# Kernel tuning notes

Measured on AMD Instinct MI355X. Metric: run time of the kernel, lower is better.

Reference implementation:

```python
import jax, jax.numpy as jnp
import numpy as np

EPS = 1e-7  # keras.backend.epsilon()
ROUTINGS = 3


def squash(s, axis=-1):
    # standard capsule squash: ||s||^2/(1+||s||^2) * s/||s||
    n2 = jnp.sum(jnp.square(s), axis=axis, keepdims=True)
    return s * (n2 / (1.0 + n2)) / jnp.sqrt(n2 + EPS)


def setup_inputs() -> dict:
    key = jax.random.key(0)
    k1, k2 = jax.random.split(key)
    B, I, K = 32, 2048, 8          # batch, input capsules, input capsule dim
    J, D = 32, 16                  # output capsules (num_capsules), dim_capsules
    x = jax.random.normal(k1, (B, I, K), dtype=jnp.float32)
    # add_weight with random_normal_initializer(stddev=0.1), shape [J, I, D, K]
    W = 0.1 * jax.random.normal(k2, (J, I, D, K), dtype=jnp.float32)
    return {"x": x, "W": W}


def reference(x, W):
    # u_ji_hat[b,j,i,d] = sum_k W[j,i,d,k] * x[b,i,k]  (the map_fn batched matmul)
    u_hat = jnp.einsum('jidk,bik->bjid', W, x)  # [B, J, I, D]
    B, J, I, D = u_hat.shape
    b = jnp.zeros((B, J, I), dtype=u_hat.dtype)  # routing logits b_ij
    v = None
    for r in range(ROUTINGS):
        c = jax.nn.softmax(b, axis=1)                 # softmax over output capsules J
        s = jnp.einsum('bji,bjid->bjd', c, u_hat)     # weighted sum over input caps i
        v = squash(s, axis=-1)                        # squash over capsule dim (axis=-2 pre-squeeze)
        if r < ROUTINGS - 1:
            # agreement = u_hat^T v : sum over capsule dim d
            b = b + jnp.einsum('bjid,bjd->bji', u_hat, v)
    return v  # [B, J, D] == tf.squeeze(v_j, [2, 4])
```

## Files before the change

### kernel.cpp

```cpp
#include <hip/hip_runtime.h>
#include <hip/hip_fp16.h>


#define ICAP    2048
#define JD      512
#define S_ELEMS 16384
#define EPSQ    1e-7f
#define NBP     256
#define ICH     8
#define WROW    1040
#define WIL     (8 * WROW)

#define GBAR_WORDS (32 + NBP * 32)

typedef _Float16 h2v __attribute__((ext_vector_type(2)));
union H8 { int4 i4; h2v h[4]; };

#if defined(__has_builtin) && __has_builtin(__builtin_amdgcn_fdot2)
#define FDOT2(a, b, c) __builtin_amdgcn_fdot2((a), (b), (c), false)
#else
__device__ inline float FDOT2(h2v a, h2v b, float c) {
    return c + (float)a[0] * (float)b[0] + (float)a[1] * (float)b[1];
}
#endif
#if defined(__has_builtin) && __has_builtin(__builtin_amdgcn_rcpf)
#define FAST_RCP(x) __builtin_amdgcn_rcpf(x)
#else
#define FAST_RCP(x) (1.0f / (x))
#endif
#if defined(__has_builtin) && __has_builtin(__builtin_amdgcn_rsqf)
#define FAST_RSQ(x) __builtin_amdgcn_rsqf(x)
#else
#define FAST_RSQ(x) rsqrtf(x)
#endif

__device__ __forceinline__ void gsync(unsigned* gb, unsigned gen,
                                      int bid, int tid) {
    __syncthreads();
    if (tid == 0) {
        __threadfence();
        __hip_atomic_store(gb + 32 + bid * 32, gen, __ATOMIC_RELAXED,
                           __HIP_MEMORY_SCOPE_AGENT);
    }
    if (bid == 0) {
        if (tid < 64) {
            const unsigned* s = gb + 32 + tid * 32;
            for (;;) {
                bool done = true;
#pragma unroll
                for (int q = 0; q < 4; ++q) {
                    const unsigned v = __hip_atomic_load(
                        s + q * 2048, __ATOMIC_RELAXED,
                        __HIP_MEMORY_SCOPE_AGENT);
                    done &= (v >= gen);
                }
                if (__all(done)) break;
                __builtin_amdgcn_s_sleep(1);
            }
            __threadfence();
            if (tid == 0)
                __hip_atomic_store(gb, gen, __ATOMIC_RELAXED,
                                   __HIP_MEMORY_SCOPE_AGENT);
        }
    } else if (tid == 0) {
        while (__hip_atomic_load(gb, __ATOMIC_RELAXED,
                                 __HIP_MEMORY_SCOPE_AGENT) < gen)
            __builtin_amdgcn_s_sleep(8);
        __threadfence();
    }
    __syncthreads();
}

__global__ __launch_bounds__(512, 1)
void caps_fused(const float4* __restrict__ Wv, const float4* __restrict__ Xv,
                float* __restrict__ vsum, __half* __restrict__ partials,
                float* __restrict__ out, unsigned* __restrict__ gbar)
{
    __shared__ __align__(16) unsigned char sWt[WIL * ICH];
    __shared__ __align__(16) unsigned char sX[4096];
    __shared__ float rbuf[8][512];

    const int tid = threadIdx.x;
    const int bid = blockIdx.x;
    const int i0  = bid * ICH;

#pragma unroll
    for (int it = 0; it < 16; ++it) {
        const int f  = it * 512 + tid;
        const int q4 = f & 31;
        const int il = (f >> 5) & 7;
        const int jj = f >> 8;
        const float4 w = Wv[((size_t)jj * ICAP + (i0 + il)) * 32 + q4];
        ushort4 h;
        h.x = __half_as_ushort(__float2half(w.x));
        h.y = __half_as_ushort(__float2half(w.y));
        h.z = __half_as_ushort(__float2half(w.z));
        h.w = __half_as_ushort(__float2half(w.w));
        const int d   = q4 >> 1;
        const int sub = q4 & 1;
        *reinterpret_cast<ushort4*>(sWt + il * WIL + (d & 7) * WROW
                                    + (2 * jj + (d >> 3)) * 16 + sub * 8) = h;
    }
    {
        const int k4 = tid & 1, il = (tid >> 1) & 7, b = tid >> 4;
        const float4 w = Xv[((size_t)b * ICAP + (i0 + il)) * 2 + k4];
        ushort4 h;
        h.x = __half_as_ushort(__float2half(w.x));
        h.y = __half_as_ushort(__float2half(w.y));
        h.z = __half_as_ushort(__float2half(w.z));
        h.w = __half_as_ushort(__float2half(w.w));
        *reinterpret_cast<ushort4*>(sX + (b * 8 + il) * 16 + k4 * 8) = h;
    }
    __syncthreads();

    const int wave = tid >> 6, lane = tid & 63;
    const int j = lane & 31, dh = lane >> 5;
    float vacc = 0.f;

#pragma unroll
    for (int r = 0; r < 3; ++r) {
        const bool first = (r == 0);
        float vs[4][8], sacc[4][8];
#pragma unroll
        for (int bb = 0; bb < 4; ++bb) {
            const int b = wave + 8 * bb;
            if (!first) {
                const float* vp = vsum + b * JD + j * 16 + dh * 8;
                const float4 a  = *reinterpret_cast<const float4*>(vp);
                const float4 bq = *reinterpret_cast<const float4*>(vp + 4);
                vs[bb][0]=a.x; vs[bb][1]=a.y; vs[bb][2]=a.z; vs[bb][3]=a.w;
                vs[bb][4]=bq.x; vs[bb][5]=bq.y; vs[bb][6]=bq.z; vs[bb][7]=bq.w;
            }
#pragma unroll
            for (int q = 0; q < 8; ++q) sacc[bb][q] = 0.f;
        }

#pragma unroll
        for (int il = 0; il < ICH; ++il) {
            H8 w8[8];
#pragma unroll
            for (int cc = 0; cc < 8; ++cc)
                w8[cc].i4 = *reinterpret_cast<const int4*>(
                    sWt + il * WIL + cc * WROW + (2 * j + dh) * 16);
#pragma unroll
            for (int bb = 0; bb < 4; ++bb) {
                const int b = wave + 8 * bb;
                H8 xv;
                xv.i4 = *reinterpret_cast<const int4*>(sX + (b * 8 + il) * 16);

                float u[8], tpart = 0.f;
#pragma unroll
                for (int q = 0; q < 8; ++q) {
                    float acc = FDOT2(w8[q].h[0], xv.h[0], 0.f);
                    acc = FDOT2(w8[q].h[1], xv.h[1], acc);
                    acc = FDOT2(w8[q].h[2], xv.h[2], acc);
                    acc = FDOT2(w8[q].h[3], xv.h[3], acc);
                    u[q] = acc;
                    if (!first) tpart = fmaf(acc, vs[bb][q], tpart);
                }
                float c;
                if (first) {
                    c = 0.03125f;
                } else {
                    const float t = tpart + __shfl_xor(tpart, 32);
                    const float e = __expf(t);
                    float se = e;
#pragma unroll
                    for (int off = 1; off <= 16; off <<= 1)
                        se += __shfl_xor(se, off);
                    c = e * FAST_RCP(se);
                }
#pragma unroll
                for (int q = 0; q < 8; ++q)
                    sacc[bb][q] = fmaf(c, u[q], sacc[bb][q]);
            }
        }

        __half* pout = partials + (size_t)bid * S_ELEMS;
#pragma unroll
        for (int bb = 0; bb < 4; ++bb) {
            const int b = wave + 8 * bb;
            union { int4 v; __half2 h[4]; } pk;
#pragma unroll
            for (int q = 0; q < 4; ++q)
                pk.h[q] = __floats2half2_rn(sacc[bb][2 * q], sacc[bb][2 * q + 1]);
            *reinterpret_cast<int4*>(pout + b * JD + j * 16 + dh * 8) = pk.v;
        }

        gsync(gbar, 2 * r + 1, bid, tid);

        {
            const int e = bid * 64 + lane;
            float s = 0.f;
            const __half* p = partials + (size_t)wave * 32 * S_ELEMS + e;
#pragma unroll
            for (int n = 0; n < 32; ++n)
                s += __half2float(p[(size_t)n * S_ELEMS]);
            rbuf[wave][lane] = s;
            __syncthreads();
            if (wave == 0) {
                s = 0.f;
#pragma unroll
                for (int k = 0; k < 8; ++k) s += rbuf[k][lane];
                float n2 = s * s;
#pragma unroll
                for (int off = 1; off <= 8; off <<= 1)
                    n2 += __shfl_xor(n2, off);
                const float scale = n2 * FAST_RCP(1.f + n2) * FAST_RSQ(n2 + EPSQ);
                const float v = s * scale;
                if (r == 2) {
                    out[e] = v;
                } else {
                    vacc += v;
                    vsum[e] = vacc;
                }
            }
        }
        if (r < 2) gsync(gbar, 2 * r + 2, bid, tid);
    }
}

extern "C" void kernel_launch(void* const* d_in, const int* in_sizes, int n_in,
                              void* d_out, int out_size, void* d_ws, size_t ws_size,
                              hipStream_t stream) {
    const float* x = (const float*)d_in[0];
    const float* W = (const float*)d_in[1];
    float* out = (float*)d_out;

    float*    vsum     = (float*)d_ws;
    __half*   partials = (__half*)((char*)d_ws + 65536);
    unsigned* gbar     = (unsigned*)((char*)partials + (size_t)NBP * S_ELEMS * 2);

    hipMemsetAsync(gbar, 0, GBAR_WORDS * sizeof(unsigned), stream);

    caps_fused<<<NBP, 512, 0, stream>>>((const float4*)W, (const float4*)x,
                                        vsum, partials, out, gbar);
}
```

Before: 176.6 us.

## Pre-convert W to fp16 tiled layout in separate kernel; spread barrier release flags

Adds a prep kernel that converts W to fp16 and writes it in the per-block shared-memory tile layout. The fused kernel can then load its tile with contiguous int4 copies instead of strided fp32 gathers with in-kernel conversion, shortening the single-wave prologue. The grid barrier release now writes 32 separate flags, each polled by a subset of blocks, which spreads the polling traffic across cache lines. The cost is an extra kernel launch plus a full read of fp32 W and a write of the fp16 copy, and W is converted on every call.

```diff
diff --git a/kernel.cpp b/kernel.cpp
--- a/kernel.cpp
+++ b/kernel.cpp
@@ -11,7 +11,7 @@
 #define WROW    1040
 #define WIL     (8 * WROW)
 
-#define GBAR_WORDS (32 + NBP * 32)
+#define GBAR_WORDS (1024 + NBP * 32)
 
 typedef _Float16 h2v __attribute__((ext_vector_type(2)));
 union H8 { int4 i4; h2v h[4]; };
@@ -34,17 +34,42 @@
 #define FAST_RSQ(x) rsqrtf(x)
 #endif
 
+__global__ __launch_bounds__(256)
+void caps_prep(const float4* __restrict__ Wv, char* __restrict__ Wt) {
+    const int t = threadIdx.x;
+    const int i = blockIdx.x * 4 + (t >> 6);
+    const int slot = t & 63;
+    const int j = slot >> 1, dh = slot & 1;
+    const float4* src = Wv + (((size_t)j * ICAP + i) * 16 + dh * 8) * 2;
+    char* dst = Wt + ((size_t)(i >> 3) * 64 + (i & 7) * 8) * 1024 + slot * 16;
+#pragma unroll
+    for (int rr = 0; rr < 8; ++rr) {
+        const float4 a = src[rr * 2];
+        const float4 b = src[rr * 2 + 1];
+        union { int4 v; ushort u[8]; } pk;
+        pk.u[0] = __half_as_ushort(__float2half(a.x));
+        pk.u[1] = __half_as_ushort(__float2half(a.y));
+        pk.u[2] = __half_as_ushort(__float2half(a.z));
+        pk.u[3] = __half_as_ushort(__float2half(a.w));
+        pk.u[4] = __half_as_ushort(__float2half(b.x));
+        pk.u[5] = __half_as_ushort(__float2half(b.y));
+        pk.u[6] = __half_as_ushort(__float2half(b.z));
+        pk.u[7] = __half_as_ushort(__float2half(b.w));
+        *reinterpret_cast<int4*>(dst + rr * 1024) = pk.v;
+    }
+}
+
 __device__ __forceinline__ void gsync(unsigned* gb, unsigned gen,
                                       int bid, int tid) {
     __syncthreads();
     if (tid == 0) {
         __threadfence();
-        __hip_atomic_store(gb + 32 + bid * 32, gen, __ATOMIC_RELAXED,
+        __hip_atomic_store(gb + 1024 + bid * 32, gen, __ATOMIC_RELAXED,
                            __HIP_MEMORY_SCOPE_AGENT);
     }
     if (bid == 0) {
         if (tid < 64) {
-            const unsigned* s = gb + 32 + tid * 32;
+            const unsigned* s = gb + 1024 + tid * 32;
             for (;;) {
                 bool done = true;
 #pragma unroll
@@ -58,21 +83,22 @@
                 __builtin_amdgcn_s_sleep(1);
             }
             __threadfence();
-            if (tid == 0)
-                __hip_atomic_store(gb, gen, __ATOMIC_RELAXED,
+            if (tid < 32)
+                __hip_atomic_store(gb + tid * 32, gen, __ATOMIC_RELAXED,
                                    __HIP_MEMORY_SCOPE_AGENT);
         }
     } else if (tid == 0) {
-        while (__hip_atomic_load(gb, __ATOMIC_RELAXED,
+        const unsigned* flag = gb + (bid & 31) * 32;
+        while (__hip_atomic_load(flag, __ATOMIC_RELAXED,
                                  __HIP_MEMORY_SCOPE_AGENT) < gen)
-            __builtin_amdgcn_s_sleep(8);
+            __builtin_amdgcn_s_sleep(16);
         __threadfence();
     }
     __syncthreads();
 }
 
 __global__ __launch_bounds__(512, 1)
-void caps_fused(const float4* __restrict__ Wv, const float4* __restrict__ Xv,
+void caps_fused(const int4* __restrict__ Wtp, const float4* __restrict__ Xv,
                 float* __restrict__ vsum, __half* __restrict__ partials,
                 float* __restrict__ out, unsigned* __restrict__ gbar)
 {
@@ -80,26 +106,20 @@
     __shared__ __align__(16) unsigned char sX[4096];
     __shared__ float rbuf[8][512];
 
-    const int tid = threadIdx.x;
-    const int bid = blockIdx.x;
-    const int i0  = bid * ICH;
-
-#pragma unroll
-    for (int it = 0; it < 16; ++it) {
-        const int f  = it * 512 + tid;
-        const int q4 = f & 31;
-        const int il = (f >> 5) & 7;
-        const int jj = f >> 8;
-        const float4 w = Wv[((size_t)jj * ICAP + (i0 + il)) * 32 + q4];
-        ushort4 h;
-        h.x = __half_as_ushort(__float2half(w.x));
-        h.y = __half_as_ushort(__float2half(w.y));
-        h.z = __half_as_ushort(__float2half(w.z));
-        h.w = __half_as_ushort(__float2half(w.w));
-        const int d   = q4 >> 1;
-        const int sub = q4 & 1;
-        *reinterpret_cast<ushort4*>(sWt + il * WIL + (d & 7) * WROW
-                                    + (2 * jj + (d >> 3)) * 16 + sub * 8) = h;
+    const int tid  = threadIdx.x;
+    const int bid  = blockIdx.x;
+    const int i0   = bid * ICH;
+    const int wave = tid >> 6, lane = tid & 63;
+
+    {
+        const int4* wsrc = Wtp + ((size_t)bid * 65536 >> 4);
+#pragma unroll
+        for (int n = 0; n < 8; ++n) {
+            const int rid = wave * 8 + n;
+            const int il = rid >> 3, rr = rid & 7;
+            const int4 v = wsrc[(size_t)rid * 64 + lane];
+            *reinterpret_cast<int4*>(sWt + il * WIL + rr * WROW + lane * 16) = v;
+        }
     }
     {
         const int k4 = tid & 1, il = (tid >> 1) & 7, b = tid >> 4;
@@ -113,7 +133,6 @@
     }
     __syncthreads();
 
-    const int wave = tid >> 6, lane = tid & 63;
     const int j = lane & 31, dh = lane >> 5;
     float vacc = 0.f;
 
@@ -230,9 +249,12 @@
     float*    vsum     = (float*)d_ws;
     __half*   partials = (__half*)((char*)d_ws + 65536);
     unsigned* gbar     = (unsigned*)((char*)partials + (size_t)NBP * S_ELEMS * 2);
+    char*     Wtp      = (char*)gbar + GBAR_WORDS * sizeof(unsigned);
 
     hipMemsetAsync(gbar, 0, GBAR_WORDS * sizeof(unsigned), stream);
 
-    caps_fused<<<NBP, 512, 0, stream>>>((const float4*)W, (const float4*)x,
+    caps_prep<<<ICAP / 4, 256, 0, stream>>>((const float4*)W, Wtp);
+
+    caps_fused<<<NBP, 512, 0, stream>>>((const int4*)Wtp, (const float4*)x,
                                         vsum, partials, out, gbar);
 }
```

Measured after the change: 190.2 us. 7.7% more time.

## Halve block count with more input capsules per block and fan out barrier flags

Applied to the files above, without the earlier changes.

Switches from 256 blocks of 8 input capsules to 128 blocks of 16, which halves the partial-sum buffer that each routing iteration writes and then reduces across blocks. The reduction is restructured so each block sums 128 elements over 128 partials using four thread groups. The grid barrier release flag is spread over 32 cache lines so waiting blocks don't all poll one word. Partial stores and loads become nontemporal. In exchange only half the CUs are used, and shared memory per block roughly doubles, which also caps occupancy.

```diff
diff --git a/kernel.cpp b/kernel.cpp
--- a/kernel.cpp
+++ b/kernel.cpp
@@ -6,14 +6,15 @@
 #define JD      512
 #define S_ELEMS 16384
 #define EPSQ    1e-7f
-#define NBP     256
-#define ICH     8
+#define NBP     128
+#define ICH     16
 #define WROW    1040
 #define WIL     (8 * WROW)
 
-#define GBAR_WORDS (32 + NBP * 32)
+#define GBAR_WORDS (1024 + NBP * 32)
 
 typedef _Float16 h2v __attribute__((ext_vector_type(2)));
+typedef int      i4v __attribute__((ext_vector_type(4)));
 union H8 { int4 i4; h2v h[4]; };
 
 #if defined(__has_builtin) && __has_builtin(__builtin_amdgcn_fdot2)
@@ -39,16 +40,16 @@
     __syncthreads();
     if (tid == 0) {
         __threadfence();
-        __hip_atomic_store(gb + 32 + bid * 32, gen, __ATOMIC_RELAXED,
+        __hip_atomic_store(gb + 1024 + bid * 32, gen, __ATOMIC_RELAXED,
                            __HIP_MEMORY_SCOPE_AGENT);
     }
     if (bid == 0) {
         if (tid < 64) {
-            const unsigned* s = gb + 32 + tid * 32;
+            const unsigned* s = gb + 1024 + tid * 32;
             for (;;) {
                 bool done = true;
 #pragma unroll
-                for (int q = 0; q < 4; ++q) {
+                for (int q = 0; q < 2; ++q) {
                     const unsigned v = __hip_atomic_load(
                         s + q * 2048, __ATOMIC_RELAXED,
                         __HIP_MEMORY_SCOPE_AGENT);
@@ -58,12 +59,13 @@
                 __builtin_amdgcn_s_sleep(1);
             }
             __threadfence();
-            if (tid == 0)
-                __hip_atomic_store(gb, gen, __ATOMIC_RELAXED,
+            if (tid < 32)
+                __hip_atomic_store(gb + tid * 32, gen, __ATOMIC_RELAXED,
                                    __HIP_MEMORY_SCOPE_AGENT);
         }
     } else if (tid == 0) {
-        while (__hip_atomic_load(gb, __ATOMIC_RELAXED,
+        const unsigned* flag = gb + (bid & 31) * 32;
+        while (__hip_atomic_load(flag, __ATOMIC_RELAXED,
                                  __HIP_MEMORY_SCOPE_AGENT) < gen)
             __builtin_amdgcn_s_sleep(8);
         __threadfence();
@@ -77,19 +79,19 @@
                 float* __restrict__ out, unsigned* __restrict__ gbar)
 {
     __shared__ __align__(16) unsigned char sWt[WIL * ICH];
-    __shared__ __align__(16) unsigned char sX[4096];
-    __shared__ float rbuf[8][512];
+    __shared__ __align__(16) unsigned char sX[8192];
+    __shared__ float rbuf[4][128];
 
     const int tid = threadIdx.x;
     const int bid = blockIdx.x;
     const int i0  = bid * ICH;
 
-#pragma unroll
-    for (int it = 0; it < 16; ++it) {
+#pragma unroll 4
+    for (int it = 0; it < 32; ++it) {
         const int f  = it * 512 + tid;
         const int q4 = f & 31;
-        const int il = (f >> 5) & 7;
-        const int jj = f >> 8;
+        const int il = (f >> 5) & 15;
+        const int jj = f >> 9;
         const float4 w = Wv[((size_t)jj * ICAP + (i0 + il)) * 32 + q4];
         ushort4 h;
         h.x = __half_as_ushort(__float2half(w.x));
@@ -101,15 +103,17 @@
         *reinterpret_cast<ushort4*>(sWt + il * WIL + (d & 7) * WROW
                                     + (2 * jj + (d >> 3)) * 16 + sub * 8) = h;
     }
-    {
-        const int k4 = tid & 1, il = (tid >> 1) & 7, b = tid >> 4;
+#pragma unroll
+    for (int it = 0; it < 2; ++it) {
+        const int f  = it * 512 + tid;
+        const int k4 = f & 1, il = (f >> 1) & 15, b = f >> 5;
         const float4 w = Xv[((size_t)b * ICAP + (i0 + il)) * 2 + k4];
         ushort4 h;
         h.x = __half_as_ushort(__float2half(w.x));
         h.y = __half_as_ushort(__float2half(w.y));
         h.z = __half_as_ushort(__float2half(w.z));
         h.w = __half_as_ushort(__float2half(w.w));
-        *reinterpret_cast<ushort4*>(sX + (b * 8 + il) * 16 + k4 * 8) = h;
+        *reinterpret_cast<ushort4*>(sX + (b * 16 + il) * 16 + k4 * 8) = h;
     }
     __syncthreads();
 
@@ -146,7 +150,7 @@
             for (int bb = 0; bb < 4; ++bb) {
                 const int b = wave + 8 * bb;
                 H8 xv;
-                xv.i4 = *reinterpret_cast<const int4*>(sX + (b * 8 + il) * 16);
+                xv.i4 = *reinterpret_cast<const int4*>(sX + (b * 16 + il) * 16);
 
                 float u[8], tpart = 0.f;
 #pragma unroll
@@ -180,28 +184,31 @@
 #pragma unroll
         for (int bb = 0; bb < 4; ++bb) {
             const int b = wave + 8 * bb;
-            union { int4 v; __half2 h[4]; } pk;
+            union { i4v v; __half2 h[4]; } pk;
 #pragma unroll
             for (int q = 0; q < 4; ++q)
                 pk.h[q] = __floats2half2_rn(sacc[bb][2 * q], sacc[bb][2 * q + 1]);
-            *reinterpret_cast<int4*>(pout + b * JD + j * 16 + dh * 8) = pk.v;
+            __builtin_nontemporal_store(
+                pk.v, reinterpret_cast<i4v*>(pout + b * JD + j * 16 + dh * 8));
         }
 
         gsync(gbar, 2 * r + 1, bid, tid);
 
         {
-            const int e = bid * 64 + lane;
+            const int eL = tid & 127;
+            const int sg = tid >> 7;
+            const int e  = bid * 128 + eL;
             float s = 0.f;
-            const __half* p = partials + (size_t)wave * 32 * S_ELEMS + e;
+            const ushort* p = reinterpret_cast<const ushort*>(partials)
+                              + (size_t)sg * 32 * S_ELEMS + e;
 #pragma unroll
             for (int n = 0; n < 32; ++n)
-                s += __half2float(p[(size_t)n * S_ELEMS]);
-            rbuf[wave][lane] = s;
+                s += __half2float(__ushort_as_half(
+                    __builtin_nontemporal_load(p + (size_t)n * S_ELEMS)));
+            rbuf[sg][eL] = s;
             __syncthreads();
-            if (wave == 0) {
-                s = 0.f;
-#pragma unroll
-                for (int k = 0; k < 8; ++k) s += rbuf[k][lane];
+            if (tid < 128) {
+                s = rbuf[0][eL] + rbuf[1][eL] + rbuf[2][eL] + rbuf[3][eL];
                 float n2 = s * s;
 #pragma unroll
                 for (int off = 1; off <= 8; off <<= 1)
@@ -231,7 +238,7 @@
     __half*   partials = (__half*)((char*)d_ws + 65536);
     unsigned* gbar     = (unsigned*)((char*)partials + (size_t)NBP * S_ELEMS * 2);
 
-    hipMemsetAsync(gbar, 0, GBAR_WORDS * sizeof(unsigned), stream);
+    (void)hipMemsetAsync(gbar, 0, GBAR_WORDS * sizeof(unsigned), stream);
 
     caps_fused<<<NBP, 512, 0, stream>>>((const float4*)W, (const float4*)x,
                                         vsum, partials, out, gbar);
```

New measurement: 411.6 us. +133.1%, slower.
